# Kernel tuning notes

Measured on AMD Instinct MI355X. Metric: run time of the kernel, lower is better.

The kernel has to match this reference:

```python
import jax, jax.numpy as jnp
import numpy as np

N_STATE = 1024
N_HEAD = 16


def setup_inputs() -> dict:
    key = jax.random.key(0)
    ks = jax.random.split(key, 8)
    B, C, H, W = 4, N_STATE, 1, 1500
    s = C ** -0.5
    return {
        "x": jax.random.normal(ks[0], (B, C, H, W), dtype=jnp.float32),
        "Wq": jax.random.normal(ks[1], (C, C), dtype=jnp.float32) * s,
        "bq": jnp.zeros((C,), dtype=jnp.float32),
        "Wk": jax.random.normal(ks[2], (C, C), dtype=jnp.float32) * s,
        "Wv": jax.random.normal(ks[3], (C, C), dtype=jnp.float32) * s,
        "bv": jnp.zeros((C,), dtype=jnp.float32),
        "Wo": jax.random.normal(ks[4], (C, C), dtype=jnp.float32) * s,
        "bo": jnp.zeros((C,), dtype=jnp.float32),
    }


def reference(x, Wq, bq, Wk, Wv, bv, Wo, bo):
    B, C, H, W = x.shape
    nh = N_HEAD
    d = C // nh
    scale = d ** -0.5

    def conv1x1(w, b=None):
        y = jnp.einsum('bchw,oc->bohw', x, w)  # 1x1 conv == per-pixel matmul
        return y if b is None else y + b[None, :, None, None]

    # [B, nh, d, H, W] per-head layout (channel split matches torch .split)
    q = conv1x1(Wq, bq).reshape(B, nh, d, H, W)
    k = conv1x1(Wk).reshape(B, nh, d, H, W)
    v = conv1x1(Wv, bv).reshape(B, nh, d, H, W)

    # attention along width axis, independently per height row and head
    scores = jnp.einsum('bndhq,bndhk->bnhqk', q, k) * scale  # [B,nh,H,Wq,Wk]
    attn = jax.nn.softmax(scores, axis=-1)                   # softmax over keys
    o = jnp.einsum('bnhqk,bndhk->bndhq', attn, v).reshape(B, C, H, W)
    return jnp.einsum('bchw,oc->bohw', o, Wo) + bo[None, :, None, None]
```

## Files before the change

kernel.cpp:

```cpp
#include <hip/hip_runtime.h>
#include <stdint.h>


typedef unsigned short u16;
typedef __bf16 bf16x8 __attribute__((ext_vector_type(8)));
typedef float  f32x4  __attribute__((ext_vector_type(4)));
typedef unsigned int __attribute__((address_space(1))) as1_uint;
typedef unsigned int __attribute__((address_space(3))) as3_uint;

__device__ __forceinline__ u16 f2bf(float f) {
    unsigned u = __float_as_uint(f);
    u += 0x7fffu + ((u >> 16) & 1u);
    return (u16)(u >> 16);
}

__device__ __forceinline__ f32x4 fzero4() { f32x4 z = {0.f, 0.f, 0.f, 0.f}; return z; }

__device__ __forceinline__ void gld16(void* lds, const void* g) {
    __builtin_amdgcn_global_load_lds((const as1_uint*)g, (as3_uint*)lds, 16, 0, 0);
}

__device__ __forceinline__ int permw(int w) {
    return (w & ~31) | ((w & 12) << 1) | ((w & 16) >> 2) | (w & 3);
}

__global__ void prep_k(const float* __restrict__ wq, const float* __restrict__ wk,
                       const float* __restrict__ wv, const float* __restrict__ wo,
                       u16* __restrict__ wb, const float* __restrict__ x,
                       u16* __restrict__ xb, u16* __restrict__ Vt) {
    __shared__ float tile[64][65];
    const int bid = blockIdx.x;
    if (bid < 4096) {
        unsigned idx = bid * 256u + threadIdx.x;
        unsigned m = idx >> 18, r = idx & 0x3ffffu;
        const float* s = (m == 0) ? wq : (m == 1) ? wk : (m == 2) ? wv : wo;
        float4 v = ((const float4*)s)[r];
        uint2 o;
        o.x = (unsigned)f2bf(v.x) | ((unsigned)f2bf(v.y) << 16);
        o.y = (unsigned)f2bf(v.z) | ((unsigned)f2bf(v.w) << 16);
        ((uint2*)(wb + (m << 20)))[r] = o;
    } else if (bid < 5632) {
        int bid2 = bid - 4096;
        const int xw = bid2 % 24, yc = (bid2 / 24) & 15, b = bid2 / 384;
        const int w0 = xw * 64, c0 = yc * 64;
        const int tw = threadIdx.x & 63, t4 = threadIdx.x >> 6;
#pragma unroll
        for (int i = 0; i < 16; i++) {
            int c = i * 4 + t4, w = w0 + tw;
            tile[c][tw] = (w < 1500) ? x[((b << 10) + c0 + c) * 1500 + w] : 0.f;
        }
        __syncthreads();
#pragma unroll
        for (int i = 0; i < 16; i++) {
            int wl = i * 4 + t4, w = w0 + wl;
            if (w < 1500) xb[((b * 1500 + w) << 10) + c0 + tw] = f2bf(tile[tw][wl]);
        }
    } else {
        const int t = threadIdx.x;
        uint2 z; z.x = 0u; z.y = 0u;
#pragma unroll
        for (int i = 0; i < 16; i++) {
            int idx = i * 256 + t;
            *(uint2*)(Vt + (long)idx * 1504 + 1500) = z;
        }
    }
}

__device__ __forceinline__ void stage32(const u16* __restrict__ A, int arow0, int amax,
                                        const u16* __restrict__ Bm, int brow0, int bmax,
                                        int k0, unsigned char* lds, int slot) {
    const int t = threadIdx.x;
    unsigned char* ab = lds + slot * 8192;
    unsigned char* bb = lds + 24576 + slot * 8192;
#pragma unroll
    for (int i = 0; i < 2; i++) {
        int xo = (i * 256 + t) << 4;
        int row = xo >> 6, seg = (xo >> 4) & 3;
        int sseg = seg ^ ((row >> 1) & 3);
        int ar = arow0 + row; if (ar > amax) ar = amax;
        int br = brow0 + row; if (br > bmax) br = bmax;
        gld16(ab + xo, A  + ((long)ar << 10) + k0 + sseg * 8);
        gld16(bb + xo, Bm + ((long)br << 10) + k0 + sseg * 8);
    }
}

__device__ __forceinline__ void gemm_core128(const u16* __restrict__ A, int arow0, int amax,
                                             const u16* __restrict__ Bm, int brow0, int bmax,
                                             f32x4 (&acc)[4][4], unsigned char* lds) {
    const int t = threadIdx.x, l15 = t & 15, lg = (t >> 4) & 3;
    const int wv = t >> 6, wm = wv >> 1, wn = wv & 1;
#pragma unroll
    for (int im = 0; im < 4; im++)
#pragma unroll
        for (int in = 0; in < 4; in++) acc[im][in] = fzero4();

    stage32(A, arow0, amax, Bm, brow0, bmax, 0, lds, 0);
    stage32(A, arow0, amax, Bm, brow0, bmax, 32, lds, 1);

    int slot = 0;
    for (int kt = 0; kt < 32; kt++) {
        if (kt < 31) asm volatile("s_waitcnt vmcnt(4)" ::: "memory");
        else         asm volatile("s_waitcnt vmcnt(0)" ::: "memory");
        __builtin_amdgcn_s_barrier();
        if (kt < 30) {
            int ns = slot + 2; if (ns >= 3) ns -= 3;
            stage32(A, arow0, amax, Bm, brow0, bmax, (kt + 2) << 5, lds, ns);
        }
        const unsigned char* ab = lds + slot * 8192;
        const unsigned char* bb = lds + 24576 + slot * 8192;
        bf16x8 af[4], bfr[4];
#pragma unroll
        for (int im = 0; im < 4; im++) {
            int row = wm * 64 + im * 16 + l15;
            af[im] = *(const bf16x8*)(ab + (row << 6) + ((lg ^ ((row >> 1) & 3)) << 4));
        }
#pragma unroll
        for (int in = 0; in < 4; in++) {
            int row = wn * 64 + in * 16 + l15;
            bfr[in] = *(const bf16x8*)(bb + (row << 6) + ((lg ^ ((row >> 1) & 3)) << 4));
        }
#pragma unroll
        for (int im = 0; im < 4; im++)
#pragma unroll
            for (int in = 0; in < 4; in++)
                acc[im][in] = __builtin_amdgcn_mfma_f32_16x16x32_bf16(af[im], bfr[in], acc[im][in], 0, 0, 0);
        slot = slot + 1; if (slot >= 3) slot = 0;
    }
}

__global__ __launch_bounds__(256, 3) void qkv_k(const u16* __restrict__ xb, const u16* __restrict__ wb,
                                                const float* __restrict__ bq, const float* __restrict__ bv,
                                                u16* __restrict__ Q, u16* __restrict__ K,
                                                u16* __restrict__ Vt) {
    __shared__ __attribute__((aligned(16))) unsigned char lds[49152];
    const int p = blockIdx.x;
    const int bid = (p & 7) * 142 + (p >> 3);
    const int t = threadIdx.x, l15 = t & 15, lg = (t >> 4) & 3;
    const int wv = t >> 6, wm = wv >> 1, wn = wv & 1;
    f32x4 acc[4][4];

    if (bid < 752) {
        const int z = bid / 376, rem = bid % 376;
        const int xt = rem % 47, yt = rem / 47;
        gemm_core128(xb, xt * 128, 5999, wb + (z << 20), yt * 128, 1023, acc, lds);
        const int m0 = xt * 128 + wm * 64, n0 = yt * 128 + wn * 64;
        u16* dst = z ? K : Q;
        const float* bias = z ? nullptr : bq;
        const float qs = z ? 1.f : 0.18033688011112042f;
#pragma unroll
        for (int im = 0; im < 4; im++) {
#pragma unroll
            for (int r = 0; r < 4; r++) {
                int tok = m0 + im * 16 + lg * 4 + r;
                if (tok < 6000) {
                    int b = tok / 1500, w = tok - b * 1500;
#pragma unroll
                    for (int in = 0; in < 4; in++) {
                        int o = n0 + in * 16 + l15;
                        float v = (acc[im][in][r] + (bias ? bias[o] : 0.f)) * qs;
                        dst[((((b << 4) + (o >> 6)) * 1500 + w) << 6) + (o & 63)] = f2bf(v);
                    }
                }
            }
        }
    } else {
        const int rem = bid - 752;
        const int xt = rem & 7, rest = rem >> 3;
        const int yt = rest % 12, b = rest / 12;
        gemm_core128(wb + (2u << 20), xt * 128, 1023, xb + b * 1500 * 1024, yt * 128, 1499, acc, lds);
        const int m0 = xt * 128 + wm * 64, n0 = yt * 128 + wn * 64;
#pragma unroll
        for (int im = 0; im < 4; im++) {
#pragma unroll
            for (int r = 0; r < 4; r++) {
                int o = m0 + im * 16 + lg * 4 + r;
                float bi = bv[o];
#pragma unroll
                for (int in = 0; in < 4; in++) {
                    int w = n0 + in * 16 + l15;
                    if (w < 1500)
                        Vt[((b << 10) + o) * 1504 + permw(w)] = f2bf(acc[im][in][r] + bi);
                }
            }
        }
    }
}

__global__ __launch_bounds__(256, 3) void gemm_out_k(const u16* __restrict__ Ow, const u16* __restrict__ wb,
                                                     const float* __restrict__ bo, float* __restrict__ out) {
    __shared__ __attribute__((aligned(16))) unsigned char lds[49152];
    const int p = blockIdx.x;
    const int lb = (p & 7) * 47 + (p >> 3);
    const int xt = lb & 7, nt = lb >> 3;
    f32x4 acc[4][4];
    gemm_core128(wb + (3u << 20), xt * 128, 1023, Ow, nt * 128, 5999, acc, lds);
    const int t = threadIdx.x, l15 = t & 15, lg = (t >> 4) & 3;
    const int wv = t >> 6, wm = wv >> 1, wn = wv & 1;
    const int m0 = xt * 128 + wm * 64;
    const int n0 = nt * 128 + wn * 64;
#pragma unroll
    for (int im = 0; im < 4; im++) {
#pragma unroll
        for (int r = 0; r < 4; r++) {
            int o = m0 + im * 16 + lg * 4 + r;
            float bi = bo[o];
#pragma unroll
            for (int in = 0; in < 4; in++) {
                int tok = n0 + in * 16 + l15;
                if (tok < 6000) {
                    int b = tok / 1500, w = tok - b * 1500;
                    out[(long)((b << 10) + o) * 1500 + w] = acc[im][in][r] + bi;
                }
            }
        }
    }
}

__global__ __launch_bounds__(512) void attn_k(const u16* __restrict__ Q, const u16* __restrict__ K,
                                              const u16* __restrict__ Vt, u16* __restrict__ O) {
    __shared__ __attribute__((aligned(16))) unsigned char lds[32768];

    const int p = blockIdx.x;
    const int lb = (p & 7) * 96 + (p >> 3);
    const int qt = lb % 12, bh = lb / 12;
    const int b = bh >> 4, h = bh & 15;
    const int t = threadIdx.x, wv = t >> 6, l15 = t & 15, g = (t >> 4) & 3;
    const int sk7 = l15 & 7;

    int q_a = qt * 128 + wv * 16 + l15; if (q_a > 1499) q_a = 1499;
    const u16* qrow = Q + (((long)bh * 1500 + q_a) << 6);
    bf16x8 qb0 = *(const bf16x8*)(qrow + (g << 3));
    bf16x8 qb1 = *(const bf16x8*)(qrow + 32 + (g << 3));

    const u16* Kbh = K + (((long)bh * 1500) << 6);
    const u16* Vtb = Vt + (long)((b << 10) + (h << 6)) * 1504;

    const int srow = t >> 3;
    const int ssw  = ((t & 7) ^ (srow & 7)) << 3;
    unsigned char* kdst = lds + (t << 4);
    unsigned char* vdst = lds + 16384 + (t << 4);

    const u16* kp_src = Kbh + ((long)srow << 6) + ssw;
    const u16* vp_src = Vtb + (long)srow * 1504 + ssw;

    f32x4 o_acc[4];
#pragma unroll
    for (int nf = 0; nf < 4; nf++) o_acc[nf] = fzero4();
    float l_part = 0.f;

    gld16(kdst, kp_src);
    gld16(vdst, vp_src);
    kp_src += 4096; vp_src += 64;
    __syncthreads();

    for (int tile = 0; tile < 24; ++tile) {
        const int cur = tile & 1;
        if (tile < 22) {
            gld16(kdst + ((cur ^ 1) << 13), kp_src);
            gld16(vdst + ((cur ^ 1) << 13), vp_src);
            kp_src += 4096; vp_src += 64;
        } else if (tile == 22) {
            int kg = 1472 + srow; if (kg > 1499) kg = 1499;
            gld16(kdst + ((cur ^ 1) << 13), Kbh + ((long)kg << 6) + ssw);
            int vc = 1472 + ssw; if (vc > 1496) vc = 1496;
            gld16(vdst + ((cur ^ 1) << 13), Vtb + (long)srow * 1504 + vc);
        }
        const unsigned char* Kl = lds + (cur << 13);
        const unsigned char* Vl = lds + 16384 + (cur << 13);

        f32x4 s[4];
        __builtin_amdgcn_s_setprio(1);
#pragma unroll
        for (int kt = 0; kt < 4; kt++) {
            const unsigned char* kp = Kl + ((kt * 16 + l15) << 7);
            bf16x8 ka0 = *(const bf16x8*)(kp + ((g ^ sk7) << 4));
            bf16x8 ka1 = *(const bf16x8*)(kp + (((g + 4) ^ sk7) << 4));
            f32x4 z = fzero4();
            z = __builtin_amdgcn_mfma_f32_16x16x32_bf16(ka0, qb0, z, 0, 0, 0);
            z = __builtin_amdgcn_mfma_f32_16x16x32_bf16(ka1, qb1, z, 0, 0, 0);
            s[kt] = z;
        }
        __builtin_amdgcn_s_setprio(0);
        if (tile == 23) {
#pragma unroll
            for (int kt = 0; kt < 4; kt++)
#pragma unroll
                for (int r = 0; r < 4; r++)
                    if (kt * 16 + g * 4 + r >= 28) s[kt][r] = -1e30f;
        }

        float pv[4][4];
        float psum = 0.f;
#pragma unroll
        for (int kt = 0; kt < 4; kt++) {
#pragma unroll
            for (int r = 0; r < 4; r++) {
                float p2 = exp2f(s[kt][r]);
                pv[kt][r] = p2;
                psum += p2;
            }
        }
        l_part += psum;

        bf16x8 pa0, pa1;
#pragma unroll
        for (int j = 0; j < 8; j++) {
            pa0[j] = (__bf16)pv[j >> 2][j & 3];
            pa1[j] = (__bf16)pv[2 + (j >> 2)][j & 3];
        }

        __builtin_amdgcn_s_setprio(1);
#pragma unroll
        for (int nf = 0; nf < 4; nf++) {
            const unsigned char* vp = Vl + ((nf * 16 + l15) << 7);
            bf16x8 vb0 = *(const bf16x8*)(vp + ((g ^ sk7) << 4));
            bf16x8 vb1 = *(const bf16x8*)(vp + (((4 + g) ^ sk7) << 4));
            o_acc[nf] = __builtin_amdgcn_mfma_f32_16x16x32_bf16(pa0, vb0, o_acc[nf], 0, 0, 0);
            o_acc[nf] = __builtin_amdgcn_mfma_f32_16x16x32_bf16(pa1, vb1, o_acc[nf], 0, 0, 0);
        }
        __builtin_amdgcn_s_setprio(0);
        __syncthreads();
    }

    l_part += __shfl_xor(l_part, 16);
    l_part += __shfl_xor(l_part, 32);
    float inv = 1.f / l_part;
#pragma unroll
    for (int r = 0; r < 4; r++) {
        float invr = __shfl(inv, g * 4 + r);
        int q = qt * 128 + wv * 16 + g * 4 + r;
        if (q < 1500) {
            u16* dst = O + ((long)(b * 1500 + q) << 10) + (h << 6);
#pragma unroll
            for (int nf = 0; nf < 4; nf++)
                dst[nf * 16 + l15] = f2bf(o_acc[nf][r] * invr);
        }
    }
}

extern "C" void kernel_launch(void* const* d_in, const int* in_sizes, int n_in,
                              void* d_out, int out_size, void* d_ws, size_t ws_size,
                              hipStream_t stream) {
    const float* x  = (const float*)d_in[0];
    const float* Wq = (const float*)d_in[1];
    const float* bq = (const float*)d_in[2];
    const float* Wk = (const float*)d_in[3];
    const float* Wv = (const float*)d_in[4];
    const float* bv = (const float*)d_in[5];
    const float* Wo = (const float*)d_in[6];
    const float* bo = (const float*)d_in[7];
    float* out = (float*)d_out;

    const size_t NEED = 57573376;
    if (ws_size < NEED) return;

    unsigned char* ws = (unsigned char*)d_ws;
    u16* xb = (u16*)(ws);
    u16* wb = (u16*)(ws + 12288000);
    u16* Qw = (u16*)(ws + 20676608);
    u16* Kw = (u16*)(ws + 32964608);
    u16* Vt = (u16*)(ws + 45252608);

    prep_k<<<dim3(5633), dim3(256), 0, stream>>>(Wq, Wk, Wv, Wo, wb, x, xb, Vt);
    qkv_k<<<dim3(1136), dim3(256), 0, stream>>>(xb, wb, bq, bv, Qw, Kw, Vt);
    attn_k<<<dim3(768), dim3(512), 0, stream>>>(Qw, Kw, Vt, xb );
    gemm_out_k<<<dim3(376), dim3(256), 0, stream>>>(xb, wb, bo, out);
}
```

Before: 168.9 us.

## Switch projection GEMMs to 256x128 tiles with 8-wave blocks and split-phase pipelining

Replaces the 128x128, 4-wave GEMM core with a 256x128 tile computed by 512-thread blocks. A is double-buffered and B is staged in halves, interleaved with MFMA phases that use s_setprio. The Q/K projections become one merged GEMM over a concatenated 2048-row weight, and V is computed over all tokens rather than per batch. XCD-aware block remapping is updated for the new grid sizes. The aim is more operand reuse per loaded byte and fewer blocks, at the cost of lower occupancy and extra barriers per k-step.

New measurement: 184.4 us. 9.2% more time.

```diff
diff --git a/kernel.cpp b/kernel.cpp
--- a/kernel.cpp
+++ b/kernel.cpp
@@ -66,27 +66,26 @@
     }
 }
 
-__device__ __forceinline__ void stage32(const u16* __restrict__ A, int arow0, int amax,
-                                        const u16* __restrict__ Bm, int brow0, int bmax,
-                                        int k0, unsigned char* lds, int slot) {
+__device__ __forceinline__ void stageAu(const u16* __restrict__ A, int arow0, int amax,
+                                        int k0, unsigned char* abuf, int u) {
     const int t = threadIdx.x;
-    unsigned char* ab = lds + slot * 8192;
-    unsigned char* bb = lds + 24576 + slot * 8192;
-#pragma unroll
-    for (int i = 0; i < 2; i++) {
-        int xo = (i * 256 + t) << 4;
-        int row = xo >> 6, seg = (xo >> 4) & 3;
-        int sseg = seg ^ ((row >> 1) & 3);
-        int ar = arow0 + row; if (ar > amax) ar = amax;
-        int br = brow0 + row; if (br > bmax) br = bmax;
-        gld16(ab + xo, A  + ((long)ar << 10) + k0 + sseg * 8);
-        gld16(bb + xo, Bm + ((long)br << 10) + k0 + sseg * 8);
-    }
-}
-
-__device__ __forceinline__ void gemm_core128(const u16* __restrict__ A, int arow0, int amax,
-                                             const u16* __restrict__ Bm, int brow0, int bmax,
-                                             f32x4 (&acc)[4][4], unsigned char* lds) {
+    int row = u * 128 + (t >> 2), seg = t & 3;
+    int sseg = seg ^ ((row >> 1) & 3);
+    int ar = arow0 + row; if (ar > amax) ar = amax;
+    gld16(abuf + u * 8192 + (t << 4), A + ((long)ar << 10) + k0 + sseg * 8);
+}
+__device__ __forceinline__ void stageB1(const u16* __restrict__ Bm, int brow0, int bmax,
+                                        int k0, unsigned char* bbuf) {
+    const int t = threadIdx.x;
+    int row = t >> 2, seg = t & 3;
+    int sseg = seg ^ ((row >> 1) & 3);
+    int br = brow0 + row; if (br > bmax) br = bmax;
+    gld16(bbuf + (t << 4), Bm + ((long)br << 10) + k0 + sseg * 8);
+}
+
+__device__ __forceinline__ void gemm_core25(const u16* __restrict__ A, int arow0, int amax,
+                                            const u16* __restrict__ Bm, int brow0, int bmax,
+                                            f32x4 (&acc)[4][4], unsigned char* lds) {
     const int t = threadIdx.x, l15 = t & 15, lg = (t >> 4) & 3;
     const int wv = t >> 6, wm = wv >> 1, wn = wv & 1;
 #pragma unroll
@@ -94,58 +93,85 @@
 #pragma unroll
         for (int in = 0; in < 4; in++) acc[im][in] = fzero4();
 
-    stage32(A, arow0, amax, Bm, brow0, bmax, 0, lds, 0);
-    stage32(A, arow0, amax, Bm, brow0, bmax, 32, lds, 1);
-
-    int slot = 0;
+    unsigned char* A0 = lds;
+    unsigned char* B0 = lds + 32768;
+
+    stageB1(Bm, brow0, bmax, 0, B0);
+    stageAu(A, arow0, amax, 0, A0, 0);
+    stageAu(A, arow0, amax, 0, A0, 1);
+    stageB1(Bm, brow0, bmax, 32, B0 + 8192);
+
     for (int kt = 0; kt < 32; kt++) {
-        if (kt < 31) asm volatile("s_waitcnt vmcnt(4)" ::: "memory");
+        const int b = kt & 1;
+        if (kt < 31) asm volatile("s_waitcnt vmcnt(1)" ::: "memory");
         else         asm volatile("s_waitcnt vmcnt(0)" ::: "memory");
         __builtin_amdgcn_s_barrier();
-        if (kt < 30) {
-            int ns = slot + 2; if (ns >= 3) ns -= 3;
-            stage32(A, arow0, amax, Bm, brow0, bmax, (kt + 2) << 5, lds, ns);
-        }
-        const unsigned char* ab = lds + slot * 8192;
-        const unsigned char* bb = lds + 24576 + slot * 8192;
-        bf16x8 af[4], bfr[4];
-#pragma unroll
-        for (int im = 0; im < 4; im++) {
-            int row = wm * 64 + im * 16 + l15;
-            af[im] = *(const bf16x8*)(ab + (row << 6) + ((lg ^ ((row >> 1) & 3)) << 4));
-        }
+        const unsigned char* Ab = A0 + (b << 14);
+        const unsigned char* Bb = B0 + (b << 13);
+
+        bf16x8 bf[4], af0, af1;
 #pragma unroll
         for (int in = 0; in < 4; in++) {
             int row = wn * 64 + in * 16 + l15;
-            bfr[in] = *(const bf16x8*)(bb + (row << 6) + ((lg ^ ((row >> 1) & 3)) << 4));
-        }
-#pragma unroll
-        for (int im = 0; im < 4; im++)
-#pragma unroll
-            for (int in = 0; in < 4; in++)
-                acc[im][in] = __builtin_amdgcn_mfma_f32_16x16x32_bf16(af[im], bfr[in], acc[im][in], 0, 0, 0);
-        slot = slot + 1; if (slot >= 3) slot = 0;
-    }
-}
-
-__global__ __launch_bounds__(256, 3) void qkv_k(const u16* __restrict__ xb, const u16* __restrict__ wb,
-                                                const float* __restrict__ bq, const float* __restrict__ bv,
-                                                u16* __restrict__ Q, u16* __restrict__ K,
-                                                u16* __restrict__ Vt) {
+            bf[in] = *(const bf16x8*)(Bb + (row << 6) + ((lg ^ ((row >> 1) & 3)) << 4));
+        }
+        {
+            int r0 = wm * 64 + l15;
+            af0 = *(const bf16x8*)(Ab + (r0 << 6) + ((lg ^ ((r0 >> 1) & 3)) << 4));
+            int r1 = wm * 64 + 16 + l15;
+            af1 = *(const bf16x8*)(Ab + (r1 << 6) + ((lg ^ ((r1 >> 1) & 3)) << 4));
+        }
+        if (kt < 31) {
+            int nk0 = (kt + 1) << 5;
+            stageAu(A, arow0, amax, nk0, A0 + ((b ^ 1) << 14), 0);
+            stageAu(A, arow0, amax, nk0, A0 + ((b ^ 1) << 14), 1);
+        }
+        __builtin_amdgcn_s_setprio(1);
+#pragma unroll
+        for (int in = 0; in < 4; in++) {
+            acc[0][in] = __builtin_amdgcn_mfma_f32_16x16x32_bf16(af0, bf[in], acc[0][in], 0, 0, 0);
+            acc[1][in] = __builtin_amdgcn_mfma_f32_16x16x32_bf16(af1, bf[in], acc[1][in], 0, 0, 0);
+        }
+        __builtin_amdgcn_s_setprio(0);
+        __builtin_amdgcn_s_barrier();
+
+        bf16x8 af2, af3;
+        {
+            int r2 = wm * 64 + 32 + l15;
+            af2 = *(const bf16x8*)(Ab + (r2 << 6) + ((lg ^ ((r2 >> 1) & 3)) << 4));
+            int r3 = wm * 64 + 48 + l15;
+            af3 = *(const bf16x8*)(Ab + (r3 << 6) + ((lg ^ ((r3 >> 1) & 3)) << 4));
+        }
+        if (kt < 30) stageB1(Bm, brow0, bmax, (kt + 2) << 5, B0 + (b << 13));
+        __builtin_amdgcn_s_setprio(1);
+#pragma unroll
+        for (int in = 0; in < 4; in++) {
+            acc[2][in] = __builtin_amdgcn_mfma_f32_16x16x32_bf16(af2, bf[in], acc[2][in], 0, 0, 0);
+            acc[3][in] = __builtin_amdgcn_mfma_f32_16x16x32_bf16(af3, bf[in], acc[3][in], 0, 0, 0);
+        }
+        __builtin_amdgcn_s_setprio(0);
+        __builtin_amdgcn_s_barrier();
+    }
+}
+
+__global__ __launch_bounds__(512) void qkv_k(const u16* __restrict__ xb, const u16* __restrict__ wb,
+                                             const float* __restrict__ bq, const float* __restrict__ bv,
+                                             u16* __restrict__ Q, u16* __restrict__ K,
+                                             u16* __restrict__ Vt) {
     __shared__ __attribute__((aligned(16))) unsigned char lds[49152];
     const int p = blockIdx.x;
-    const int bid = (p & 7) * 142 + (p >> 3);
+    const int xcd = p & 7, idx = p >> 3;
+    const int bid = (xcd < 4 ? xcd * 72 : 288 + (xcd - 4) * 71) + idx;
     const int t = threadIdx.x, l15 = t & 15, lg = (t >> 4) & 3;
     const int wv = t >> 6, wm = wv >> 1, wn = wv & 1;
     f32x4 acc[4][4];
 
-    if (bid < 752) {
-        const int z = bid / 376, rem = bid % 376;
-        const int xt = rem % 47, yt = rem / 47;
-        gemm_core128(xb, xt * 128, 5999, wb + (z << 20), yt * 128, 1023, acc, lds);
-        const int m0 = xt * 128 + wm * 64, n0 = yt * 128 + wn * 64;
+    if (bid < 384) {
+        const int xt = bid % 24, yt = bid / 24;
+        gemm_core25(xb, xt * 256, 5999, wb, yt * 128, 2047, acc, lds);
+        const int m0 = xt * 256 + wm * 64, n0 = yt * 128 + wn * 64;
+        const int z = yt >> 3;
         u16* dst = z ? K : Q;
-        const float* bias = z ? nullptr : bq;
         const float qs = z ? 1.f : 0.18033688011112042f;
 #pragma unroll
         for (int im = 0; im < 4; im++) {
@@ -156,19 +182,18 @@
                     int b = tok / 1500, w = tok - b * 1500;
 #pragma unroll
                     for (int in = 0; in < 4; in++) {
-                        int o = n0 + in * 16 + l15;
-                        float v = (acc[im][in][r] + (bias ? bias[o] : 0.f)) * qs;
+                        int o = (n0 + in * 16 + l15) & 1023;
+                        float v = (acc[im][in][r] + (z ? 0.f : bq[o])) * qs;
                         dst[((((b << 4) + (o >> 6)) * 1500 + w) << 6) + (o & 63)] = f2bf(v);
                     }
                 }
             }
         }
     } else {
-        const int rem = bid - 752;
-        const int xt = rem & 7, rest = rem >> 3;
-        const int yt = rest % 12, b = rest / 12;
-        gemm_core128(wb + (2u << 20), xt * 128, 1023, xb + b * 1500 * 1024, yt * 128, 1499, acc, lds);
-        const int m0 = xt * 128 + wm * 64, n0 = yt * 128 + wn * 64;
+        const int rem = bid - 384;
+        const int xt = rem & 3, nt = rem >> 2;
+        gemm_core25(wb + (2u << 20), xt * 256, 1023, xb, nt * 128, 5999, acc, lds);
+        const int m0 = xt * 256 + wm * 64, n0 = nt * 128 + wn * 64;
 #pragma unroll
         for (int im = 0; im < 4; im++) {
 #pragma unroll
@@ -177,27 +202,29 @@
                 float bi = bv[o];
 #pragma unroll
                 for (int in = 0; in < 4; in++) {
-                    int w = n0 + in * 16 + l15;
-                    if (w < 1500)
+                    int tok = n0 + in * 16 + l15;
+                    if (tok < 6000) {
+                        int b = tok / 1500, w = tok - b * 1500;
                         Vt[((b << 10) + o) * 1504 + permw(w)] = f2bf(acc[im][in][r] + bi);
+                    }
                 }
             }
         }
     }
 }
 
-__global__ __launch_bounds__(256, 3) void gemm_out_k(const u16* __restrict__ Ow, const u16* __restrict__ wb,
-                                                     const float* __restrict__ bo, float* __restrict__ out) {
+__global__ __launch_bounds__(512) void gemm_out_k(const u16* __restrict__ Ow, const u16* __restrict__ wb,
+                                                  const float* __restrict__ bo, float* __restrict__ out) {
     __shared__ __attribute__((aligned(16))) unsigned char lds[49152];
     const int p = blockIdx.x;
-    const int lb = (p & 7) * 47 + (p >> 3);
-    const int xt = lb & 7, nt = lb >> 3;
-    f32x4 acc[4][4];
-    gemm_core128(wb + (3u << 20), xt * 128, 1023, Ow, nt * 128, 5999, acc, lds);
+    const int xcd = p & 7, idx = p >> 3;
+    const int lb = (xcd < 4 ? xcd * 24 : 96 + (xcd - 4) * 23) + idx;
+    const int xt = lb & 3, nt = lb >> 2;
     const int t = threadIdx.x, l15 = t & 15, lg = (t >> 4) & 3;
     const int wv = t >> 6, wm = wv >> 1, wn = wv & 1;
-    const int m0 = xt * 128 + wm * 64;
-    const int n0 = nt * 128 + wn * 64;
+    f32x4 acc[4][4];
+    gemm_core25(wb + (3u << 20), xt * 256, 1023, Ow, nt * 128, 5999, acc, lds);
+    const int m0 = xt * 256 + wm * 64, n0 = nt * 128 + wn * 64;
 #pragma unroll
     for (int im = 0; im < 4; im++) {
 #pragma unroll
@@ -362,7 +389,7 @@
     u16* Vt = (u16*)(ws + 45252608);
 
     prep_k<<<dim3(5633), dim3(256), 0, stream>>>(Wq, Wk, Wv, Wo, wb, x, xb, Vt);
-    qkv_k<<<dim3(1136), dim3(256), 0, stream>>>(xb, wb, bq, bv, Qw, Kw, Vt);
+    qkv_k<<<dim3(572), dim3(512), 0, stream>>>(xb, wb, bq, bv, Qw, Kw, Vt);
     attn_k<<<dim3(768), dim3(512), 0, stream>>>(Qw, Kw, Vt, xb );
-    gemm_out_k<<<dim3(376), dim3(256), 0, stream>>>(xb, wb, bo, out);
-}
+    gemm_out_k<<<dim3(188), dim3(512), 0, stream>>>(xb, wb, bo, out);
+}
```

## Widen QKV GEMM tiles to 128x256 and fuse Q/K weight tiles

Applied to the files above, without the earlier changes.

Replaces the 128x128 QKV GEMM with a 128x256 tile variant that holds a 4x8 accumulator per wave and a larger three-slot LDS ring. Q and K are computed as one 2048-wide output so each x tile is loaded once for 256 output channels. The V GEMM now tiles across all batches' tokens with a clamped row bound instead of per-batch 1500-wide tiles. The block count halves to 568 and occupancy drops to 2 blocks per CU, trading less load traffic and more MFMA work per LDS read against higher register and LDS pressure.

Result: slower. 186.3 us (+10.3%).

```diff
diff --git a/kernel.cpp b/kernel.cpp
--- a/kernel.cpp
+++ b/kernel.cpp
@@ -128,24 +128,89 @@
     }
 }
 
-__global__ __launch_bounds__(256, 3) void qkv_k(const u16* __restrict__ xb, const u16* __restrict__ wb,
+__device__ __forceinline__ void stage_w(const u16* __restrict__ A, int arow0, int amax,
+                                        const u16* __restrict__ Bm, int brow0, int bmax,
+                                        int k0, unsigned char* lds, int slot) {
+    const int t = threadIdx.x;
+    unsigned char* ab = lds + slot * 8192;
+    unsigned char* bb = lds + 24576 + slot * 16384;
+#pragma unroll
+    for (int i = 0; i < 2; i++) {
+        int xo = (i * 256 + t) << 4;
+        int row = xo >> 6, seg = (xo >> 4) & 3;
+        int sseg = seg ^ ((row >> 1) & 3);
+        int ar = arow0 + row; if (ar > amax) ar = amax;
+        gld16(ab + xo, A + ((long)ar << 10) + k0 + sseg * 8);
+    }
+#pragma unroll
+    for (int i = 0; i < 4; i++) {
+        int xo = (i * 256 + t) << 4;
+        int row = xo >> 6, seg = (xo >> 4) & 3;
+        int sseg = seg ^ ((row >> 1) & 3);
+        int br = brow0 + row; if (br > bmax) br = bmax;
+        gld16(bb + xo, Bm + ((long)br << 10) + k0 + sseg * 8);
+    }
+}
+
+__device__ __forceinline__ void gemm_core_w(const u16* __restrict__ A, int arow0, int amax,
+                                            const u16* __restrict__ Bm, int brow0, int bmax,
+                                            f32x4 (&acc)[4][8], unsigned char* lds) {
+    const int t = threadIdx.x, l15 = t & 15, lg = (t >> 4) & 3;
+    const int wv = t >> 6, wm = wv >> 1, wn = wv & 1;
+#pragma unroll
+    for (int im = 0; im < 4; im++)
+#pragma unroll
+        for (int in = 0; in < 8; in++) acc[im][in] = fzero4();
+
+    stage_w(A, arow0, amax, Bm, brow0, bmax, 0, lds, 0);
+    stage_w(A, arow0, amax, Bm, brow0, bmax, 32, lds, 1);
+
+    int slot = 0;
+    for (int kt = 0; kt < 32; kt++) {
+        if (kt < 31) asm volatile("s_waitcnt vmcnt(6)" ::: "memory");
+        else         asm volatile("s_waitcnt vmcnt(0)" ::: "memory");
+        __builtin_amdgcn_s_barrier();
+        if (kt < 30) {
+            int ns = slot + 2; if (ns >= 3) ns -= 3;
+            stage_w(A, arow0, amax, Bm, brow0, bmax, (kt + 2) << 5, lds, ns);
+        }
+        const unsigned char* ab = lds + slot * 8192;
+        const unsigned char* bb = lds + 24576 + slot * 16384;
+        bf16x8 bfr[8];
+#pragma unroll
+        for (int in = 0; in < 8; in++) {
+            int row = wn * 128 + in * 16 + l15;
+            bfr[in] = *(const bf16x8*)(bb + (row << 6) + ((lg ^ ((row >> 1) & 3)) << 4));
+        }
+#pragma unroll
+        for (int im = 0; im < 4; im++) {
+            int row = wm * 64 + im * 16 + l15;
+            bf16x8 af = *(const bf16x8*)(ab + (row << 6) + ((lg ^ ((row >> 1) & 3)) << 4));
+#pragma unroll
+            for (int in = 0; in < 8; in++)
+                acc[im][in] = __builtin_amdgcn_mfma_f32_16x16x32_bf16(af, bfr[in], acc[im][in], 0, 0, 0);
+        }
+        slot = slot + 1; if (slot >= 3) slot = 0;
+    }
+}
+
+__global__ __launch_bounds__(256, 2) void qkv_k(const u16* __restrict__ xb, const u16* __restrict__ wb,
                                                 const float* __restrict__ bq, const float* __restrict__ bv,
                                                 u16* __restrict__ Q, u16* __restrict__ K,
                                                 u16* __restrict__ Vt) {
-    __shared__ __attribute__((aligned(16))) unsigned char lds[49152];
+    __shared__ __attribute__((aligned(16))) unsigned char lds[73728];
     const int p = blockIdx.x;
-    const int bid = (p & 7) * 142 + (p >> 3);
+    const int bid = (p & 7) * 71 + (p >> 3);
     const int t = threadIdx.x, l15 = t & 15, lg = (t >> 4) & 3;
     const int wv = t >> 6, wm = wv >> 1, wn = wv & 1;
-    f32x4 acc[4][4];
-
-    if (bid < 752) {
-        const int z = bid / 376, rem = bid % 376;
-        const int xt = rem % 47, yt = rem / 47;
-        gemm_core128(xb, xt * 128, 5999, wb + (z << 20), yt * 128, 1023, acc, lds);
-        const int m0 = xt * 128 + wm * 64, n0 = yt * 128 + wn * 64;
+    f32x4 acc[4][8];
+
+    if (bid < 376) {
+        const int xt = bid % 47, yt = bid / 47;
+        gemm_core_w(xb, xt * 128, 5999, wb, yt * 256, 2047, acc, lds);
+        const int m0 = xt * 128 + wm * 64, n0 = yt * 256 + wn * 128;
+        const int z = yt >> 2;
         u16* dst = z ? K : Q;
-        const float* bias = z ? nullptr : bq;
         const float qs = z ? 1.f : 0.18033688011112042f;
 #pragma unroll
         for (int im = 0; im < 4; im++) {
@@ -155,20 +220,19 @@
                 if (tok < 6000) {
                     int b = tok / 1500, w = tok - b * 1500;
 #pragma unroll
-                    for (int in = 0; in < 4; in++) {
-                        int o = n0 + in * 16 + l15;
-                        float v = (acc[im][in][r] + (bias ? bias[o] : 0.f)) * qs;
+                    for (int in = 0; in < 8; in++) {
+                        int o = (n0 + in * 16 + l15) & 1023;
+                        float v = (acc[im][in][r] + (z ? 0.f : bq[o])) * qs;
                         dst[((((b << 4) + (o >> 6)) * 1500 + w) << 6) + (o & 63)] = f2bf(v);
                     }
                 }
             }
         }
     } else {
-        const int rem = bid - 752;
-        const int xt = rem & 7, rest = rem >> 3;
-        const int yt = rest % 12, b = rest / 12;
-        gemm_core128(wb + (2u << 20), xt * 128, 1023, xb + b * 1500 * 1024, yt * 128, 1499, acc, lds);
-        const int m0 = xt * 128 + wm * 64, n0 = yt * 128 + wn * 64;
+        const int rem = bid - 376;
+        const int xt = rem & 7, nt = rem >> 3;
+        gemm_core_w(wb + (2u << 20), xt * 128, 1023, xb, nt * 256, 5999, acc, lds);
+        const int m0 = xt * 128 + wm * 64, n0 = nt * 256 + wn * 128;
 #pragma unroll
         for (int im = 0; im < 4; im++) {
 #pragma unroll
@@ -176,10 +240,12 @@
                 int o = m0 + im * 16 + lg * 4 + r;
                 float bi = bv[o];
 #pragma unroll
-                for (int in = 0; in < 4; in++) {
-                    int w = n0 + in * 16 + l15;
-                    if (w < 1500)
+                for (int in = 0; in < 8; in++) {
+                    int tok = n0 + in * 16 + l15;
+                    if (tok < 6000) {
+                        int b = tok / 1500, w = tok - b * 1500;
                         Vt[((b << 10) + o) * 1504 + permw(w)] = f2bf(acc[im][in][r] + bi);
+                    }
                 }
             }
         }
@@ -362,7 +428,7 @@
     u16* Vt = (u16*)(ws + 45252608);
 
     prep_k<<<dim3(5633), dim3(256), 0, stream>>>(Wq, Wk, Wv, Wo, wb, x, xb, Vt);
-    qkv_k<<<dim3(1136), dim3(256), 0, stream>>>(xb, wb, bq, bv, Qw, Kw, Vt);
+    qkv_k<<<dim3(568), dim3(256), 0, stream>>>(xb, wb, bq, bv, Qw, Kw, Vt);
     attn_k<<<dim3(768), dim3(512), 0, stream>>>(Qw, Kw, Vt, xb );
     gemm_out_k<<<dim3(376), dim3(256), 0, stream>>>(xb, wb, bo, out);
 }
```
